# Performance work log

Hardware: AMD Instinct MI355X
Metric: run time of the kernel (lower is better)

## Reference

```python
import jax, jax.numpy as jnp
import numpy as np

B, T, E, H = 4, 2048, 1024, 16
HS = E // H  # 64
EPS = 1e-5


def _layernorm(x, g, b):
    mu = jnp.mean(x, axis=-1, keepdims=True)
    var = jnp.mean(jnp.square(x - mu), axis=-1, keepdims=True)
    return (x - mu) * jax.lax.rsqrt(var + EPS) * g + b


def setup_inputs() -> dict:
    key = jax.random.key(0)
    ks = jax.random.split(key, 12)
    s = 0.02
    return {
        "x": jax.random.normal(ks[0], (B, T, E), dtype=jnp.float32),
        "ln1_g": jnp.ones((E,), jnp.float32),
        "ln1_b": jnp.zeros((E,), jnp.float32),
        "Wq": jax.random.normal(ks[1], (H, E, HS), jnp.float32) * s,
        "Wk": jax.random.normal(ks[2], (H, E, HS), jnp.float32) * s,
        "Wv": jax.random.normal(ks[3], (H, E, HS), jnp.float32) * s,
        "Wo": jax.random.normal(ks[4], (E, E), jnp.float32) * s,
        "bo": jnp.zeros((E,), jnp.float32),
        "ln2_g": jnp.ones((E,), jnp.float32),
        "ln2_b": jnp.zeros((E,), jnp.float32),
        "W1": jax.random.normal(ks[5], (E, 4 * E), jnp.float32) * s,
        "b1": jnp.zeros((4 * E,), jnp.float32),
        "W2": jax.random.normal(ks[6], (4 * E, E), jnp.float32) * s,
        "b2": jnp.zeros((E,), jnp.float32),
    }


def reference(x, ln1_g, ln1_b, Wq, Wk, Wv, Wo, bo, ln2_g, ln2_b, W1, b1, W2, b2):
    # --- self-attention (pre-LN) ---
    h = _layernorm(x, ln1_g, ln1_b)                      # [B,T,E]
    q = jnp.einsum('bte,hed->bhtd', h, Wq)               # [B,H,T,HS]
    k = jnp.einsum('bte,hed->bhtd', h, Wk)
    v = jnp.einsum('bte,hed->bhtd', h, Wv)
    scores = jnp.einsum('bhtd,bhsd->bhts', q, k) * (HS ** -0.5)  # [B,H,T,T]
    att = jax.nn.softmax(scores, axis=-1)
    o = jnp.einsum('bhts,bhsd->bhtd', att, v)            # [B,H,T,HS]
    o = jnp.transpose(o, (0, 2, 1, 3)).reshape(B, T, E)  # concat heads
    x = x + o @ Wo + bo                                  # residual
    # --- feed-forward (pre-LN) ---
    h2 = _layernorm(x, ln2_g, ln2_b)
    x = x + jax.nn.relu(h2 @ W1 + b1) @ W2 + b2
    return x
```

## Files before the change

kernel.cpp:

```cpp
#include <hip/hip_runtime.h>
#include <stdint.h>


typedef __attribute__((ext_vector_type(8))) short s16x8;
typedef __attribute__((ext_vector_type(4))) float f32x4;
typedef unsigned short u16;
typedef __attribute__((ext_vector_type(4))) unsigned short u16x4;

#define XSW(r) ((((r) & 7) ^ (((r) >> 3) & 7)) << 4)

__device__ __forceinline__ u16 f2bf(float f) {
    uint32_t u = __float_as_uint(f);
    u += 0x7fffu + ((u >> 16) & 1u);
    return (u16)(u >> 16);
}
__device__ __forceinline__ float bf2f(u16 u) {
    return __uint_as_float(((uint32_t)u) << 16);
}
__device__ __forceinline__ uint32_t pk2(float a, float b) {
    return (uint32_t)f2bf(a) | ((uint32_t)f2bf(b) << 16);
}

__device__ __forceinline__ void gld16(const void* g, void* l) {
    __builtin_amdgcn_global_load_lds(
        (const __attribute__((address_space(1))) unsigned int*)g,
        (__attribute__((address_space(3))) unsigned int*)l, 16, 0, 0);
}

__global__ __launch_bounds__(256)
void ln_bf16(const float* __restrict__ x, const float* __restrict__ g,
             const float* __restrict__ bta, u16* __restrict__ y) {
    __shared__ float red[8];
    const int row = blockIdx.x;
    const int t = threadIdx.x;
    const float4 xv = ((const float4*)(x + (size_t)row * 1024))[t];
    float s = xv.x + xv.y + xv.z + xv.w;
    float q = xv.x*xv.x + xv.y*xv.y + xv.z*xv.z + xv.w*xv.w;
#pragma unroll
    for (int off = 32; off; off >>= 1) {
        s += __shfl_down(s, off, 64);
        q += __shfl_down(q, off, 64);
    }
    if ((t & 63) == 0) { red[(t>>6)*2] = s; red[(t>>6)*2+1] = q; }
    __syncthreads();
    const float st = red[0]+red[2]+red[4]+red[6];
    const float qt = red[1]+red[3]+red[5]+red[7];
    const float mu = st * (1.f/1024.f);
    const float rs = rsqrtf(qt*(1.f/1024.f) - mu*mu + 1e-5f);
    const float4 gv = ((const float4*)g)[t];
    const float4 bv = ((const float4*)bta)[t];
    u16x4 o;
    o.x = f2bf((xv.x-mu)*rs*gv.x + bv.x);
    o.y = f2bf((xv.y-mu)*rs*gv.y + bv.y);
    o.z = f2bf((xv.z-mu)*rs*gv.z + bv.z);
    o.w = f2bf((xv.w-mu)*rs*gv.w + bv.w);
    ((u16x4*)(y + (size_t)row*1024))[t] = o;
}

__global__ __launch_bounds__(256)
void transpose_f32_bf16(const float* __restrict__ in, u16* __restrict__ out,
                        int K, int N) {
    __shared__ float tile[64][65];
    const int k0 = blockIdx.x * 64;
    const int n0 = blockIdx.y * 64;
    const int t = threadIdx.x;
    const int r = t >> 2;
    const int c = (t & 3) * 16;
    const float* ip = in + (size_t)(k0 + r) * N + n0 + c;
#pragma unroll
    for (int i = 0; i < 4; ++i) {
        const float4 v = *(const float4*)(ip + i*4);
        tile[r][c+i*4+0]=v.x; tile[r][c+i*4+1]=v.y;
        tile[r][c+i*4+2]=v.z; tile[r][c+i*4+3]=v.w;
    }
    __syncthreads();
    u16 tmp[16] __attribute__((aligned(16)));
#pragma unroll
    for (int i = 0; i < 16; ++i) tmp[i] = f2bf(tile[c+i][r]);
    u16* op = out + (size_t)(n0 + r) * K + k0 + c;
    *(s16x8*)op       = *(const s16x8*)&tmp[0];
    *(s16x8*)(op + 8) = *(const s16x8*)&tmp[8];
}

__global__ __launch_bounds__(256)
void pack_wcat(const float* __restrict__ Wq, const float* __restrict__ Wk,
               const float* __restrict__ Wv, u16* __restrict__ out) {
    __shared__ float tile[64][65];
    const int ph = blockIdx.y;
    const int p = ph >> 4, h = ph & 15;
    const float* W = (p == 0) ? Wq : (p == 1 ? Wk : Wv);
    const float* in = W + (size_t)h * 64 * 1024;
    const int k0 = blockIdx.x * 64;
    const int t = threadIdx.x;
    const int r = t >> 2;
    const int c = (t & 3) * 16;
    const float* ip = in + (size_t)(k0 + r) * 64 + c;
#pragma unroll
    for (int i = 0; i < 4; ++i) {
        const float4 v = *(const float4*)(ip + i*4);
        tile[r][c+i*4+0]=v.x; tile[r][c+i*4+1]=v.y;
        tile[r][c+i*4+2]=v.z; tile[r][c+i*4+3]=v.w;
    }
    __syncthreads();
    u16 tmp[16] __attribute__((aligned(16)));
#pragma unroll
    for (int i = 0; i < 16; ++i) tmp[i] = f2bf(tile[c+i][r]);
    u16* op = out + (size_t)(p*1024 + h*64 + r) * 1024 + k0 + c;
    *(s16x8*)op       = *(const s16x8*)&tmp[0];
    *(s16x8*)(op + 8) = *(const s16x8*)&tmp[8];
}

template<bool RELU, bool HAS_BIAS, bool HAS_RES, bool OUT_BF16>
__global__ __launch_bounds__(256)
void bgemm(const u16* __restrict__ A, int lda,
           const u16* __restrict__ Bt, int ldb,
           void* Cv, int ldc,
           const float* __restrict__ bias,
           const float* Res, int ldres, int K)
{
    __shared__ u16 Als[128*64];
    __shared__ u16 Bls[128*64];
    const int tid = threadIdx.x;
    const int wid = tid >> 6, lane = tid & 63;
    const int bm = blockIdx.y * 128, bn = blockIdx.x * 128;
    const int wr = (wid >> 1) * 64, wc = (wid & 1) * 64;
    const int fr = lane & 15, fq = lane >> 4;
    const int sr8 = lane >> 3, sc8 = (lane & 7) * 8;

    const f32x4 zero = {0.f, 0.f, 0.f, 0.f};
    f32x4 acc[4][4];
#pragma unroll
    for (int m = 0; m < 4; ++m)
#pragma unroll
        for (int n = 0; n < 4; ++n) acc[m][n] = zero;

    const u16* Ap = A  + (size_t)(bm + wid*32 + sr8) * lda + sc8;
    const u16* Bp = Bt + (size_t)(bn + wid*32 + sr8) * ldb + sc8;
    u16* Alp = Als + wid*2048 + lane*8;
    u16* Blp = Bls + wid*2048 + lane*8;

    for (int k0 = 0; k0 < K; k0 += 64) {
#pragma unroll
        for (int c = 0; c < 4; ++c) {
            gld16(Ap + (size_t)(c*8)*lda + k0, Alp + c*512);
            gld16(Bp + (size_t)(c*8)*ldb + k0, Blp + c*512);
        }
        __syncthreads();
#pragma unroll
        for (int kk = 0; kk < 2; ++kk) {
            s16x8 af[4], bf[4];
#pragma unroll
            for (int m = 0; m < 4; ++m)
                af[m] = *(const s16x8*)((const char*)Als + (wr+m*16+fr)*128 + kk*64 + fq*16);
#pragma unroll
            for (int n = 0; n < 4; ++n)
                bf[n] = *(const s16x8*)((const char*)Bls + (wc+n*16+fr)*128 + kk*64 + fq*16);
#pragma unroll
            for (int m = 0; m < 4; ++m)
#pragma unroll
                for (int n = 0; n < 4; ++n)
                    acc[m][n] = __builtin_amdgcn_mfma_f32_16x16x32_bf16(
                        af[m], bf[n], acc[m][n], 0, 0, 0);
        }
        __syncthreads();
    }

    float* Cf = (float*)Cv;
    u16*  Cb = (u16*)Cv;
#pragma unroll
    for (int n = 0; n < 4; ++n) {
        const int col = bn + wc + n*16 + fr;
        const float bval = HAS_BIAS ? bias[col] : 0.f;
#pragma unroll
        for (int m = 0; m < 4; ++m) {
#pragma unroll
            for (int j = 0; j < 4; ++j) {
                const int row = bm + wr + m*16 + fq*4 + j;
                float v = acc[m][n][j] + bval;
                if (HAS_RES) v += Res[(size_t)row * ldres + col];
                if (RELU)    v = fmaxf(v, 0.f);
                if (OUT_BF16) Cb[(size_t)row * ldc + col] = f2bf(v);
                else          Cf[(size_t)row * ldc + col] = v;
            }
        }
    }
}

__global__ __launch_bounds__(256)
void attn_bf16(const u16* __restrict__ qkv, u16* __restrict__ out) {
    __shared__ u16 Ks[128*64];
    __shared__ u16 Vt[64*128];
    __shared__ u16 Ps[4][16*128];
    const int b = blockIdx.y >> 4, h = blockIdx.y & 15;
    const int q0 = blockIdx.x << 6;
    const int tid = threadIdx.x;
    const int wid = tid >> 6, lane = tid & 63;
    const int fr = lane & 15, fq = lane >> 4;
    const int srow = tid >> 2;
    const int sce  = (tid & 3) * 16;
    const size_t tokbase = (size_t)b * 2048;
    const f32x4 zero = {0.f, 0.f, 0.f, 0.f};

    u16* Qst = (u16*)Ps;
    {
        const u16* qp = qkv + (tokbase + q0 + srow)*3072 + h*64 + sce;
        const s16x8 v0 = *(const s16x8*)qp;
        const s16x8 v1 = *(const s16x8*)(qp + 8);
        *(s16x8*)((char*)Qst + srow*128 + ((sce*2)      ^ XSW(srow))) = v0;
        *(s16x8*)((char*)Qst + srow*128 + ((sce*2 + 16) ^ XSW(srow))) = v1;
    }
    __syncthreads();
    s16x8 qf[2];
    {
        const int qrow = wid*16 + fr;
#pragma unroll
        for (int kk = 0; kk < 2; ++kk) {
            const s16x8 raw = *(const s16x8*)((const char*)Qst + qrow*128
                                 + ((kk*64 + fq*16) ^ XSW(qrow)));
#pragma unroll
            for (int i = 0; i < 8; ++i)
                qf[kk][i] = (short)f2bf(bf2f((u16)raw[i]) * 0.125f);
        }
    }

    float m_run = -1e30f, l_run = 0.f;
    f32x4 oacc[4];
#pragma unroll
    for (int nd = 0; nd < 4; ++nd) oacc[nd] = zero;

    for (int kt = 0; kt < 2048; kt += 128) {
        const u16* kp0 = qkv + (tokbase + kt + srow)*3072 + 1024 + h*64 + sce;
        const u16* kp1 = kp0 + (size_t)64*3072;
        const s16x8 ka0 = *(const s16x8*)kp0;
        const s16x8 ka1 = *(const s16x8*)(kp0 + 8);
        const s16x8 kb0 = *(const s16x8*)kp1;
        const s16x8 kb1 = *(const s16x8*)(kp1 + 8);
        const s16x8 va0 = *(const s16x8*)(kp0 + 1024);
        const s16x8 va1 = *(const s16x8*)(kp0 + 1032);
        const s16x8 vb0 = *(const s16x8*)(kp1 + 1024);
        const s16x8 vb1 = *(const s16x8*)(kp1 + 1032);
        __syncthreads();
        {
            const int r0 = srow, r1 = srow + 64;
            *(s16x8*)((char*)Ks + r0*128 + ((sce*2)      ^ XSW(r0))) = ka0;
            *(s16x8*)((char*)Ks + r0*128 + ((sce*2 + 16) ^ XSW(r0))) = ka1;
            *(s16x8*)((char*)Ks + r1*128 + ((sce*2)      ^ XSW(r1))) = kb0;
            *(s16x8*)((char*)Ks + r1*128 + ((sce*2 + 16) ^ XSW(r1))) = kb1;
        }
#pragma unroll
        for (int i = 0; i < 8; ++i) {
            const int d0 = sce + i, d1 = sce + 8 + i;
            *(u16*)((char*)Vt + d0*256 + ((srow*2)        ^ XSW(d0))) = (u16)va0[i];
            *(u16*)((char*)Vt + d1*256 + ((srow*2)        ^ XSW(d1))) = (u16)va1[i];
            *(u16*)((char*)Vt + d0*256 + (((srow+64)*2)   ^ XSW(d0))) = (u16)vb0[i];
            *(u16*)((char*)Vt + d1*256 + (((srow+64)*2)   ^ XSW(d1))) = (u16)vb1[i];
        }
        __syncthreads();

        f32x4 sv[8];
#pragma unroll
        for (int n = 0; n < 8; ++n) {
            sv[n] = zero;
            const int r = n*16 + fr;
#pragma unroll
            for (int kk = 0; kk < 2; ++kk) {
                const s16x8 kf = *(const s16x8*)((const char*)Ks + r*128
                                     + ((kk*64 + fq*16) ^ XSW(r)));
                sv[n] = __builtin_amdgcn_mfma_f32_16x16x32_bf16(kf, qf[kk], sv[n], 0,0,0);
            }
        }

        float pv[32];
        float mx = -1e30f;
#pragma unroll
        for (int n = 0; n < 8; ++n)
#pragma unroll
            for (int j = 0; j < 4; ++j) {
                const float s = sv[n][j];
                pv[n*4 + j] = s;
                mx = fmaxf(mx, s);
            }
        mx = fmaxf(mx, __shfl_xor(mx, 16, 64));
        mx = fmaxf(mx, __shfl_xor(mx, 32, 64));
        const float mn = fmaxf(m_run, mx);
        const float al = __expf(m_run - mn);
        m_run = mn;
        float rs = 0.f;
#pragma unroll
        for (int t = 0; t < 32; ++t) { pv[t] = __expf(pv[t] - mn); rs += pv[t]; }
        rs += __shfl_xor(rs, 16, 64);
        rs += __shfl_xor(rs, 32, 64);
        l_run = l_run * al + rs;
#pragma unroll
        for (int nd = 0; nd < 4; ++nd)
#pragma unroll
            for (int j = 0; j < 4; ++j) oacc[nd][j] *= al;

        u16* Pw = (u16*)Ps + wid*2048;
#pragma unroll
        for (int n = 0; n < 8; ++n) {
            const uint64_t w = (uint64_t)pk2(pv[n*4+0], pv[n*4+1])
                             | ((uint64_t)pk2(pv[n*4+2], pv[n*4+3]) << 32);
            *(uint64_t*)((char*)Pw + fr*256 + ((n*32 + fq*8) ^ XSW(fr))) = w;
        }
        asm volatile("s_waitcnt lgkmcnt(0)" ::: "memory");
        __builtin_amdgcn_sched_barrier(0);

        s16x8 pf[4];
#pragma unroll
        for (int k2 = 0; k2 < 4; ++k2)
            pf[k2] = *(const s16x8*)((const char*)Pw + fr*256
                         + ((k2*64 + fq*16) ^ XSW(fr)));
#pragma unroll
        for (int nd = 0; nd < 4; ++nd) {
            const int d = nd*16 + fr;
#pragma unroll
            for (int k2 = 0; k2 < 4; ++k2) {
                const s16x8 vf = *(const s16x8*)((const char*)Vt + d*256
                                     + ((k2*64 + fq*16) ^ XSW(d)));
                oacc[nd] = __builtin_amdgcn_mfma_f32_16x16x32_bf16(vf, pf[k2], oacc[nd], 0,0,0);
            }
        }
    }

    const float inv = 1.0f / l_run;
    const size_t row = tokbase + q0 + wid*16 + fr;
#pragma unroll
    for (int nd = 0; nd < 4; ++nd) {
        u16x4 o;
#pragma unroll
        for (int j = 0; j < 4; ++j) o[j] = f2bf(oacc[nd][j] * inv);
        *(u16x4*)(out + row*1024 + h*64 + nd*16 + fq*4) = o;
    }
}

extern "C" void kernel_launch(void* const* d_in, const int* in_sizes, int n_in,
                              void* d_out, int out_size, void* d_ws, size_t ws_size,
                              hipStream_t stream) {
    (void)in_sizes; (void)n_in; (void)out_size; (void)ws_size;
    const float* x     = (const float*)d_in[0];
    const float* ln1_g = (const float*)d_in[1];
    const float* ln1_b = (const float*)d_in[2];
    const float* Wq    = (const float*)d_in[3];
    const float* Wk    = (const float*)d_in[4];
    const float* Wv    = (const float*)d_in[5];
    const float* Wo    = (const float*)d_in[6];
    const float* bo    = (const float*)d_in[7];
    const float* ln2_g = (const float*)d_in[8];
    const float* ln2_b = (const float*)d_in[9];
    const float* W1    = (const float*)d_in[10];
    const float* b1    = (const float*)d_in[11];
    const float* W2    = (const float*)d_in[12];
    const float* b2    = (const float*)d_in[13];
    float* out = (float*)d_out;

    char* w = (char*)d_ws;
    u16* WcatT = (u16*)w;  w += (size_t)3072*1024*2;
    u16* WoT   = (u16*)w;  w += (size_t)1024*1024*2;
    u16* W1T   = (u16*)w;  w += (size_t)4096*1024*2;
    u16* W2T   = (u16*)w;  w += (size_t)1024*4096*2;
    u16* hb    = (u16*)w;  w += (size_t)8192*1024*2;
    u16* qkvb  = (u16*)w;  w += (size_t)8192*3072*2;
    u16* attno = (u16*)w;  w += (size_t)8192*1024*2;
    u16* a1    = (u16*)w;  w += (size_t)8192*4096*2;

    pack_wcat<<<dim3(16, 48), 256, 0, stream>>>(Wq, Wk, Wv, WcatT);
    transpose_f32_bf16<<<dim3(16, 16), 256, 0, stream>>>(Wo, WoT, 1024, 1024);
    transpose_f32_bf16<<<dim3(16, 64), 256, 0, stream>>>(W1, W1T, 1024, 4096);
    transpose_f32_bf16<<<dim3(64, 16), 256, 0, stream>>>(W2, W2T, 4096, 1024);

    ln_bf16<<<dim3(8192), 256, 0, stream>>>(x, ln1_g, ln1_b, hb);
    bgemm<false,false,false,true><<<dim3(24, 64), 256, 0, stream>>>(
        hb, 1024, WcatT, 1024, qkvb, 3072, nullptr, nullptr, 0, 1024);
    attn_bf16<<<dim3(32, 64), 256, 0, stream>>>(qkvb, attno);
    bgemm<false,true,true,false><<<dim3(8, 64), 256, 0, stream>>>(
        attno, 1024, WoT, 1024, out, 1024, bo, x, 1024, 1024);
    ln_bf16<<<dim3(8192), 256, 0, stream>>>(out, ln2_g, ln2_b, hb);
    bgemm<true,true,false,true><<<dim3(32, 64), 256, 0, stream>>>(
        hb, 1024, W1T, 1024, a1, 4096, b1, nullptr, 0, 1024);
    bgemm<false,true,true,false><<<dim3(8, 64), 256, 0, stream>>>(
        a1, 4096, W2T, 4096, out, 1024, b2, out, 1024, 4096);
}
```

Before: 634.6 us.

## Write V pre-transposed from QKV GEMM and prefetch K/V tiles in attention

The QKV GEMM epilogue now writes the V columns straight into a per-head transposed [b,h,d,t] buffer, while Q and K go to a narrower 2048-wide buffer. The attention kernel can then load V with vector stores into LDS instead of scattered 2-byte transposing writes. The K/V tile for the next step is register-prefetched during the current step's compute. The kernel also folds log2(e) into the Q scale to use the raw v_exp_f32 instruction, and raises wave priority around the MFMA loops. The risk is that the transposed V stores in the GEMM epilogue are strided, 2-byte and uncoalesced, which may slow that GEMM.

```diff
diff --git a/kernel.cpp b/kernel.cpp
--- a/kernel.cpp
+++ b/kernel.cpp
@@ -19,6 +19,11 @@
 }
 __device__ __forceinline__ uint32_t pk2(float a, float b) {
     return (uint32_t)f2bf(a) | ((uint32_t)f2bf(b) << 16);
+}
+__device__ __forceinline__ float exp2_fast(float x) {
+    float r;
+    asm("v_exp_f32 %0, %1" : "=v"(r) : "v"(x));
+    return r;
 }
 
 __device__ __forceinline__ void gld16(const void* g, void* l) {
@@ -110,13 +115,14 @@
     *(s16x8*)(op + 8) = *(const s16x8*)&tmp[8];
 }
 
-template<bool RELU, bool HAS_BIAS, bool HAS_RES, bool OUT_BF16>
+template<bool RELU, bool HAS_BIAS, bool HAS_RES, bool OUT_BF16, bool SPLIT_V>
 __global__ __launch_bounds__(256)
 void bgemm(const u16* __restrict__ A, int lda,
            const u16* __restrict__ Bt, int ldb,
            void* Cv, int ldc,
            const float* __restrict__ bias,
-           const float* Res, int ldres, int K)
+           const float* Res, int ldres, int K,
+           u16* __restrict__ vT)
 {
     __shared__ u16 Als[128*64];
     __shared__ u16 Bls[128*64];
@@ -167,6 +173,23 @@
 
     float* Cf = (float*)Cv;
     u16*  Cb = (u16*)Cv;
+    if (SPLIT_V && bn >= 2048) {
+#pragma unroll
+        for (int n = 0; n < 4; ++n) {
+            const int local = bn + wc + n*16 + fr - 2048;
+            const int hh = local >> 6, dd = local & 63;
+#pragma unroll
+            for (int m = 0; m < 4; ++m) {
+#pragma unroll
+                for (int j = 0; j < 4; ++j) {
+                    const int row = bm + wr + m*16 + fq*4 + j;
+                    const int bb = row >> 11, tt = row & 2047;
+                    vT[((size_t)(bb*16 + hh)*64 + dd)*2048 + tt] = f2bf(acc[m][n][j]);
+                }
+            }
+        }
+        return;
+    }
 #pragma unroll
     for (int n = 0; n < 4; ++n) {
         const int col = bn + wc + n*16 + fr;
@@ -187,7 +210,8 @@
 }
 
 __global__ __launch_bounds__(256)
-void attn_bf16(const u16* __restrict__ qkv, u16* __restrict__ out) {
+void attn_bf16(const u16* __restrict__ qk, const u16* __restrict__ vT,
+               u16* __restrict__ out) {
     __shared__ u16 Ks[128*64];
     __shared__ u16 Vt[64*128];
     __shared__ u16 Ps[4][16*128];
@@ -198,12 +222,15 @@
     const int fr = lane & 15, fq = lane >> 4;
     const int srow = tid >> 2;
     const int sce  = (tid & 3) * 16;
+    const int vd   = tid >> 4;
+    const int vt0  = (tid & 15) * 8;
     const size_t tokbase = (size_t)b * 2048;
+    const u16* vbase = vT + (size_t)(b*16 + h) * 64 * 2048;
     const f32x4 zero = {0.f, 0.f, 0.f, 0.f};
 
     u16* Qst = (u16*)Ps;
     {
-        const u16* qp = qkv + (tokbase + q0 + srow)*3072 + h*64 + sce;
+        const u16* qp = qk + (tokbase + q0 + srow)*2048 + h*64 + sce;
         const s16x8 v0 = *(const s16x8*)qp;
         const s16x8 v1 = *(const s16x8*)(qp + 8);
         *(s16x8*)((char*)Qst + srow*128 + ((sce*2)      ^ XSW(srow))) = v0;
@@ -213,13 +240,14 @@
     s16x8 qf[2];
     {
         const int qrow = wid*16 + fr;
+        const float qscale = 0.125f * 1.44269504f;
 #pragma unroll
         for (int kk = 0; kk < 2; ++kk) {
             const s16x8 raw = *(const s16x8*)((const char*)Qst + qrow*128
                                  + ((kk*64 + fq*16) ^ XSW(qrow)));
 #pragma unroll
             for (int i = 0; i < 8; ++i)
-                qf[kk][i] = (short)f2bf(bf2f((u16)raw[i]) * 0.125f);
+                qf[kk][i] = (short)f2bf(bf2f((u16)raw[i]) * qscale);
         }
     }
 
@@ -228,36 +256,48 @@
 #pragma unroll
     for (int nd = 0; nd < 4; ++nd) oacc[nd] = zero;
 
+    s16x8 kr[4], vr[4];
+    {
+        const u16* kp0 = qk + (tokbase + srow)*2048 + 1024 + h*64 + sce;
+        kr[0] = *(const s16x8*)kp0;
+        kr[1] = *(const s16x8*)(kp0 + 8);
+        kr[2] = *(const s16x8*)(kp0 + (size_t)64*2048);
+        kr[3] = *(const s16x8*)(kp0 + (size_t)64*2048 + 8);
+#pragma unroll
+        for (int c = 0; c < 4; ++c)
+            vr[c] = *(const s16x8*)(vbase + (size_t)(vd + 16*c)*2048 + vt0);
+    }
+
     for (int kt = 0; kt < 2048; kt += 128) {
-        const u16* kp0 = qkv + (tokbase + kt + srow)*3072 + 1024 + h*64 + sce;
-        const u16* kp1 = kp0 + (size_t)64*3072;
-        const s16x8 ka0 = *(const s16x8*)kp0;
-        const s16x8 ka1 = *(const s16x8*)(kp0 + 8);
-        const s16x8 kb0 = *(const s16x8*)kp1;
-        const s16x8 kb1 = *(const s16x8*)(kp1 + 8);
-        const s16x8 va0 = *(const s16x8*)(kp0 + 1024);
-        const s16x8 va1 = *(const s16x8*)(kp0 + 1032);
-        const s16x8 vb0 = *(const s16x8*)(kp1 + 1024);
-        const s16x8 vb1 = *(const s16x8*)(kp1 + 1032);
         __syncthreads();
         {
             const int r0 = srow, r1 = srow + 64;
-            *(s16x8*)((char*)Ks + r0*128 + ((sce*2)      ^ XSW(r0))) = ka0;
-            *(s16x8*)((char*)Ks + r0*128 + ((sce*2 + 16) ^ XSW(r0))) = ka1;
-            *(s16x8*)((char*)Ks + r1*128 + ((sce*2)      ^ XSW(r1))) = kb0;
-            *(s16x8*)((char*)Ks + r1*128 + ((sce*2 + 16) ^ XSW(r1))) = kb1;
-        }
-#pragma unroll
-        for (int i = 0; i < 8; ++i) {
-            const int d0 = sce + i, d1 = sce + 8 + i;
-            *(u16*)((char*)Vt + d0*256 + ((srow*2)        ^ XSW(d0))) = (u16)va0[i];
-            *(u16*)((char*)Vt + d1*256 + ((srow*2)        ^ XSW(d1))) = (u16)va1[i];
-            *(u16*)((char*)Vt + d0*256 + (((srow+64)*2)   ^ XSW(d0))) = (u16)vb0[i];
-            *(u16*)((char*)Vt + d1*256 + (((srow+64)*2)   ^ XSW(d1))) = (u16)vb1[i];
+            *(s16x8*)((char*)Ks + r0*128 + ((sce*2)      ^ XSW(r0))) = kr[0];
+            *(s16x8*)((char*)Ks + r0*128 + ((sce*2 + 16) ^ XSW(r0))) = kr[1];
+            *(s16x8*)((char*)Ks + r1*128 + ((sce*2)      ^ XSW(r1))) = kr[2];
+            *(s16x8*)((char*)Ks + r1*128 + ((sce*2 + 16) ^ XSW(r1))) = kr[3];
+        }
+#pragma unroll
+        for (int c = 0; c < 4; ++c) {
+            const int d = vd + 16*c;
+            *(s16x8*)((char*)Vt + d*256 + ((vt0*2) ^ XSW(d))) = vr[c];
         }
         __syncthreads();
 
+        if (kt + 128 < 2048) {
+            const u16* kp0 = qk + (tokbase + kt + 128 + srow)*2048 + 1024 + h*64 + sce;
+            kr[0] = *(const s16x8*)kp0;
+            kr[1] = *(const s16x8*)(kp0 + 8);
+            kr[2] = *(const s16x8*)(kp0 + (size_t)64*2048);
+            kr[3] = *(const s16x8*)(kp0 + (size_t)64*2048 + 8);
+#pragma unroll
+            for (int c = 0; c < 4; ++c)
+                vr[c] = *(const s16x8*)(vbase + (size_t)(vd + 16*c)*2048
+                                        + kt + 128 + vt0);
+        }
+
         f32x4 sv[8];
+        __builtin_amdgcn_s_setprio(1);
 #pragma unroll
         for (int n = 0; n < 8; ++n) {
             sv[n] = zero;
@@ -269,6 +309,7 @@
                 sv[n] = __builtin_amdgcn_mfma_f32_16x16x32_bf16(kf, qf[kk], sv[n], 0,0,0);
             }
         }
+        __builtin_amdgcn_s_setprio(0);
 
         float pv[32];
         float mx = -1e30f;
@@ -283,11 +324,11 @@
         mx = fmaxf(mx, __shfl_xor(mx, 16, 64));
         mx = fmaxf(mx, __shfl_xor(mx, 32, 64));
         const float mn = fmaxf(m_run, mx);
-        const float al = __expf(m_run - mn);
+        const float al = exp2_fast(m_run - mn);
         m_run = mn;
         float rs = 0.f;
 #pragma unroll
-        for (int t = 0; t < 32; ++t) { pv[t] = __expf(pv[t] - mn); rs += pv[t]; }
+        for (int t = 0; t < 32; ++t) { pv[t] = exp2_fast(pv[t] - mn); rs += pv[t]; }
         rs += __shfl_xor(rs, 16, 64);
         rs += __shfl_xor(rs, 32, 64);
         l_run = l_run * al + rs;
@@ -311,6 +352,7 @@
         for (int k2 = 0; k2 < 4; ++k2)
             pf[k2] = *(const s16x8*)((const char*)Pw + fr*256
                          + ((k2*64 + fq*16) ^ XSW(fr)));
+        __builtin_amdgcn_s_setprio(1);
 #pragma unroll
         for (int nd = 0; nd < 4; ++nd) {
             const int d = nd*16 + fr;
@@ -321,6 +363,7 @@
                 oacc[nd] = __builtin_amdgcn_mfma_f32_16x16x32_bf16(vf, pf[k2], oacc[nd], 0,0,0);
             }
         }
+        __builtin_amdgcn_s_setprio(0);
     }
 
     const float inv = 1.0f / l_run;
@@ -360,7 +403,8 @@
     u16* W1T   = (u16*)w;  w += (size_t)4096*1024*2;
     u16* W2T   = (u16*)w;  w += (size_t)1024*4096*2;
     u16* hb    = (u16*)w;  w += (size_t)8192*1024*2;
-    u16* qkvb  = (u16*)w;  w += (size_t)8192*3072*2;
+    u16* qkb   = (u16*)w;  w += (size_t)8192*2048*2;
+    u16* vTb   = (u16*)w;  w += (size_t)64*64*2048*2;
     u16* attno = (u16*)w;  w += (size_t)8192*1024*2;
     u16* a1    = (u16*)w;  w += (size_t)8192*4096*2;
 
@@ -370,14 +414,14 @@
     transpose_f32_bf16<<<dim3(64, 16), 256, 0, stream>>>(W2, W2T, 4096, 1024);
 
     ln_bf16<<<dim3(8192), 256, 0, stream>>>(x, ln1_g, ln1_b, hb);
-    bgemm<false,false,false,true><<<dim3(24, 64), 256, 0, stream>>>(
-        hb, 1024, WcatT, 1024, qkvb, 3072, nullptr, nullptr, 0, 1024);
-    attn_bf16<<<dim3(32, 64), 256, 0, stream>>>(qkvb, attno);
-    bgemm<false,true,true,false><<<dim3(8, 64), 256, 0, stream>>>(
-        attno, 1024, WoT, 1024, out, 1024, bo, x, 1024, 1024);
+    bgemm<false,false,false,true,true><<<dim3(24, 64), 256, 0, stream>>>(
+        hb, 1024, WcatT, 1024, qkb, 2048, nullptr, nullptr, 0, 1024, vTb);
+    attn_bf16<<<dim3(32, 64), 256, 0, stream>>>(qkb, vTb, attno);
+    bgemm<false,true,true,false,false><<<dim3(8, 64), 256, 0, stream>>>(
+        attno, 1024, WoT, 1024, out, 1024, bo, x, 1024, 1024, nullptr);
     ln_bf16<<<dim3(8192), 256, 0, stream>>>(out, ln2_g, ln2_b, hb);
-    bgemm<true,true,false,true><<<dim3(32, 64), 256, 0, stream>>>(
-        hb, 1024, W1T, 1024, a1, 4096, b1, nullptr, 0, 1024);
-    bgemm<false,true,true,false><<<dim3(8, 64), 256, 0, stream>>>(
-        a1, 4096, W2T, 4096, out, 1024, b2, out, 1024, 4096);
-}
+    bgemm<true,true,false,true,false><<<dim3(32, 64), 256, 0, stream>>>(
+        hb, 1024, W1T, 1024, a1, 4096, b1, nullptr, 0, 1024, nullptr);
+    bgemm<false,true,true,false,false><<<dim3(8, 64), 256, 0, stream>>>(
+        a1, 4096, W2T, 4096, out, 1024, b2, out, 1024, 4096, nullptr);
+}
```

Result: no change. 640.5 us (+0.9%).
